# Kernel tuning notes

Hardware: AMD Instinct MI355X
Metric: run time of the kernel (lower is better)

## Reference

```python
import jax, jax.numpy as jnp
import numpy as np

B, N, C, H = 2, 2048, 1024, 16
D = C // H          # head_dim = 64
HALF = D // 2       # 32 complex pairs per head


def setup_inputs() -> dict:
    key = jax.random.key(0)
    k1, k2, k3, k4 = jax.random.split(key, 4)
    x = jax.random.normal(k1, (B, N, C), dtype=jnp.float32)
    # 0.02 init scale keeps softmax logits in a sane range
    qkv_w = jax.random.normal(k2, (3 * C, C), dtype=jnp.float32) * 0.02
    proj_w = jax.random.normal(k3, (C, C), dtype=jnp.float32) * 0.02
    proj_b = jax.random.normal(k4, (C,), dtype=jnp.float32) * 0.02
    # standard RoPE frequencies: theta = 10000^{-2i/D}
    inv_freq = 1.0 / (10000.0 ** (jnp.arange(0, D, 2, dtype=jnp.float32) / D))
    angles = jnp.arange(N, dtype=jnp.float32)[:, None] * inv_freq[None, :]  # [N, HALF]
    return {
        "x": x, "qkv_w": qkv_w, "proj_w": proj_w, "proj_b": proj_b,
        "freqs_cos": jnp.cos(angles), "freqs_sin": jnp.sin(angles),
    }


def _rope(t, cos, sin):
    # t: [B, N, H, D]; cos/sin: [N, HALF] -> broadcast as [1, N, 1, HALF]
    tr = t.reshape(B, N, H, HALF, 2)
    t_re, t_im = tr[..., 0], tr[..., 1]
    c = cos[None, :, None, :]
    s = sin[None, :, None, :]
    o_re = t_re * c - t_im * s
    o_im = t_re * s + t_im * c
    return jnp.stack([o_re, o_im], axis=-1).reshape(B, N, H, D)


def reference(x, qkv_w, proj_w, proj_b, freqs_cos, freqs_sin):
    scale = D ** -0.5
    qkv = x @ qkv_w.T                              # [B, N, 3C] (no bias: qkv_bias=False)
    qkv = qkv.reshape(B, N, 3, H, D)
    q, k, v = qkv[:, :, 0], qkv[:, :, 1], qkv[:, :, 2]  # [B, N, H, D]
    q = _rope(q, freqs_cos, freqs_sin)
    k = _rope(k, freqs_cos, freqs_sin)
    scores = jnp.einsum("bqhd,bkhd->bhqk", q, k) * scale
    attn = jax.nn.softmax(scores, axis=-1)         # dropout p=0.0 -> identity
    out = jnp.einsum("bhqk,bkhd->bqhd", attn, v).reshape(B, N, C)
    return out @ proj_w.T + proj_b
```

## Files before the change

### kernel.cpp

```cpp
#include <hip/hip_runtime.h>
#include <hip/hip_bf16.h>

#define B_ 2
#define N_ 2048
#define C_ 1024
#define H_ 16
#define D_ 64
#define HALF_ 32

typedef __attribute__((ext_vector_type(8))) __bf16 bf16x8;
typedef __attribute__((ext_vector_type(8))) unsigned short u16x8;
typedef __attribute__((ext_vector_type(4))) float f32x4;
typedef __attribute__((ext_vector_type(16))) float f32x16;

__device__ __forceinline__ unsigned short f2bf(float f) {
  union { float f; unsigned u; } v; v.f = f;
  unsigned r = v.u + 0x7FFFu + ((v.u >> 16) & 1u);
  return (unsigned short)(r >> 16);
}

__device__ __forceinline__ unsigned cvt_pk_bf16(float lo, float hi) {
  unsigned r;
  asm("v_cvt_pk_bf16_f32 %0, %1, %2" : "=v"(r) : "v"(lo), "v"(hi));
  return r;
}

__device__ __forceinline__ void gload_lds16(const void* g, void* l) {
  __builtin_amdgcn_global_load_lds(
      (const __attribute__((address_space(1))) void*)g,
      (__attribute__((address_space(3))) void*)l, 16, 0, 0);
}

__global__ __launch_bounds__(256) void cast3_f32_bf16(
    const float* __restrict__ a, const float* __restrict__ b,
    const float* __restrict__ c, unsigned short* __restrict__ oa,
    unsigned short* __restrict__ ob, unsigned short* __restrict__ oc,
    const float* __restrict__ cosT, const float* __restrict__ sinT,
    float2* __restrict__ csT) {
  int i = blockIdx.x * 256 + threadIdx.x;
  if (i >= 2097152) {
    int i2 = i - 2097152;
    csT[i2] = make_float2(cosT[i2], sinT[i2]);
    return;
  }
  const float4* src;
  ushort4* dst;
  int off;
  if (i < 1048576) {
    src = (const float4*)a; dst = (ushort4*)oa; off = i;
  } else if (i < 1835008) {
    src = (const float4*)b; dst = (ushort4*)ob; off = i - 1048576;
  } else {
    src = (const float4*)c; dst = (ushort4*)oc; off = i - 1835008;
  }
  float4 v = src[off];
  ushort4 o;
  o.x = f2bf(v.x); o.y = f2bf(v.y); o.z = f2bf(v.z); o.w = f2bf(v.w);
  dst[off] = o;
}

template <int EPI>
__global__ __launch_bounds__(256) void gemm_bt(
    const unsigned short* __restrict__ A, const unsigned short* __restrict__ Bw,
    int M, int Nn, int K,
    float* __restrict__ Cout, const float* __restrict__ bias,
    unsigned short* __restrict__ qo, unsigned short* __restrict__ ko,
    unsigned short* __restrict__ vto,
    const float2* __restrict__ csT) {
  __shared__ __align__(16) unsigned short As[2][128][64];
  __shared__ __align__(16) unsigned short Bs[2][128][64];
  const int tid = threadIdx.x;
  const int lane = tid & 63;
  const int wid = tid >> 6;
  const int wm = wid >> 1, wn = wid & 1;
  const int l15 = lane & 15;
  const int g = lane >> 4;

  const int per = gridDim.x >> 3;
  const int f = blockIdx.x;
  const int nat = (f & 7) * per + (f >> 3);
  const int mtiles = M >> 7;
  const int m0 = (nat % mtiles) * 128;
  const int n0 = (nat / mtiles) * 128;

  const int srow = wid * 8 + (lane >> 3);
  const int scol = ((lane & 7) ^ ((lane >> 3) & 7)) * 8;
  const int b7r = l15 & 7;

  auto stage = [&](int kt, int buf) {
#pragma unroll
    for (int j = 0; j < 4; ++j) {
      gload_lds16(&A[(size_t)(m0 + j * 32 + srow) * K + kt * 64 + scol],
                  &As[buf][j * 32 + wid * 8][0]);
      gload_lds16(&Bw[(size_t)(n0 + j * 32 + srow) * K + kt * 64 + scol],
                  &Bs[buf][j * 32 + wid * 8][0]);
    }
  };

  f32x4 acc[4][4] = {};

  const int nK = K >> 6;
  stage(0, 0);
  stage(1, 1);

  for (int kt = 0; kt < nK; ++kt) {
    const int buf = kt & 1;
    if (kt == nK - 1) asm volatile("s_waitcnt vmcnt(0)" ::: "memory");
    else              asm volatile("s_waitcnt vmcnt(8)" ::: "memory");
    __builtin_amdgcn_s_barrier();
    __builtin_amdgcn_sched_barrier(0);
#pragma unroll
    for (int kk = 0; kk < 2; ++kk) {
      bf16x8 af[4], bfv[4];
#pragma unroll
      for (int m = 0; m < 4; ++m)
        af[m] = *reinterpret_cast<const bf16x8*>(
            &As[buf][wm * 64 + m * 16 + l15][((kk * 4 + g) ^ b7r) * 8]);
#pragma unroll
      for (int n = 0; n < 4; ++n)
        bfv[n] = *reinterpret_cast<const bf16x8*>(
            &Bs[buf][wn * 64 + n * 16 + l15][((kk * 4 + g) ^ b7r) * 8]);
#pragma unroll
      for (int m = 0; m < 4; ++m)
#pragma unroll
        for (int n = 0; n < 4; ++n)
          acc[m][n] = __builtin_amdgcn_mfma_f32_16x16x32_bf16(af[m], bfv[n], acc[m][n], 0, 0, 0);
    }
    __builtin_amdgcn_s_barrier();
    if (kt + 2 < nK) stage(kt + 2, buf);
  }

  if constexpr (EPI == 0) {
#pragma unroll
    for (int n = 0; n < 4; ++n) {
      int col = n0 + wn * 64 + n * 16 + l15;
      float bv = bias[col];
#pragma unroll
      for (int m = 0; m < 4; ++m) {
        int rbase = m0 + wm * 64 + m * 16 + (lane >> 4) * 4;
#pragma unroll
        for (int r = 0; r < 4; ++r)
          Cout[(size_t)(rbase + r) * Nn + col] = acc[m][n][r] + bv;
      }
    }
  } else {
    const int which = n0 >> 10;
    if (which == 2) {
#pragma unroll
      for (int m = 0; m < 4; ++m)
#pragma unroll
        for (int n = 0; n < 4; ++n) {
          int col = n0 + wn * 64 + n * 16 + l15;
          int hc = col & 1023;
          int hh = hc >> 6, d = hc & 63;
          int row0 = m0 + wm * 64 + m * 16 + g * 4;
          int seq0 = row0 & (N_ - 1), bb = row0 >> 11;
          int seqP = (seq0 & ~12) | ((seq0 & 4) << 1) | ((seq0 & 8) >> 1);
          ushort4 pk;
          pk.x = f2bf(acc[m][n][0]); pk.y = f2bf(acc[m][n][1]);
          pk.z = f2bf(acc[m][n][2]); pk.w = f2bf(acc[m][n][3]);
          *reinterpret_cast<ushort4*>(
              &vto[(((size_t)bb * H_ + hh) * D_ + d) * N_ + seqP]) = pk;
        }
    } else {
      unsigned short* dst = (which == 0) ? qo : ko;
      const float qscale = (which == 0) ? 0.125f * 1.44269504f : 1.0f;
#pragma unroll
      for (int m = 0; m < 4; ++m)
#pragma unroll
        for (int n = 0; n < 4; ++n)
#pragma unroll
          for (int r = 0; r < 4; ++r) {
            int col = n0 + wn * 64 + n * 16 + l15;
            int row = m0 + wm * 64 + m * 16 + g * 4 + r;
            float val = acc[m][n][r];
            float partner = __shfl_xor(val, 1);
            int hc = col & 1023;
            int hh = hc >> 6, d = hc & 63;
            int seq = row & (N_ - 1), bb = row >> 11;
            float2 cs = csT[seq * HALF_ + (d >> 1)];
            float res = (d & 1) ? (partner * cs.y + val * cs.x) : (val * cs.x - partner * cs.y);
            res *= qscale;
            dst[(((size_t)bb * H_ + hh) * N_ + seq) * D_ + d] = f2bf(res);
          }
    }
  }
}

__global__ __launch_bounds__(512) void attn_kernel(
    const unsigned short* __restrict__ q,
    const unsigned short* __restrict__ k,
    const unsigned short* __restrict__ vt,
    unsigned short* __restrict__ o) {
  __shared__ __align__(16) unsigned short Kl[2][64][64];
  __shared__ __align__(16) unsigned short Vl[2][64][64];

  const int tid = threadIdx.x;
  const int lane = tid & 63;
  const int w = tid >> 6;
  const int l31 = lane & 31;
  const int hi = lane >> 5;

  const int bid = blockIdx.x;
  const int nat = (bid & 7) * 32 + (bid >> 3);
  const int qt = nat & 7;
  const int bh = nat >> 3;
  const int b = bh >> 4, h = bh & 15;

  const size_t hk = (size_t)bh * N_ * D_;
  const size_t hv = (size_t)bh * D_ * N_;
  const int qrow = qt * 256 + w * 32 + l31;

  bf16x8 qf[4];
#pragma unroll
  for (int kt = 0; kt < 4; ++kt)
    qf[kt] = *reinterpret_cast<const bf16x8*>(
        &q[hk + (size_t)qrow * D_ + kt * 16 + hi * 8]);

  const int prow = tid >> 3;
  const int pchk = tid & 7;
  const int swz = (pchk ^ (prow & 7)) * 8;

  u16x8 kr, vr;
  auto issueK = [&](int t) {
    kr = *reinterpret_cast<const u16x8*>(&k[hk + (size_t)(t * 64 + prow) * D_ + pchk * 8]);
  };
  auto issueV = [&](int t) {
    vr = *reinterpret_cast<const u16x8*>(&vt[hv + (size_t)prow * N_ + t * 64 + pchk * 8]);
  };
  auto commitK = [&](int buf) { *reinterpret_cast<u16x8*>(&Kl[buf][prow][swz]) = kr; };
  auto commitV = [&](int buf) { *reinterpret_cast<u16x8*>(&Vl[buf][prow][swz]) = vr; };

  f32x16 accO[2] = {};
  float lrun = 0.f;
  const int b7 = l31 & 7;
  const int NT = N_ / 64;

  f32x16 sA[2], sB[2];

#define QK_MFMA(T, SC)                                                        \
  do {                                                                        \
    f32x16 z_ = {};                                                           \
    SC[0] = z_; SC[1] = z_;                                                   \
    __builtin_amdgcn_s_setprio(1);                                            \
    _Pragma("unroll")                                                         \
    for (int kb = 0; kb < 2; ++kb)                                            \
      _Pragma("unroll")                                                       \
      for (int kt = 0; kt < 4; ++kt) {                                        \
        bf16x8 kf = *reinterpret_cast<const bf16x8*>(                         \
            &Kl[(T) & 1][kb * 32 + l31][(((kt * 2 + hi) ^ b7)) * 8]);         \
        SC[kb] = __builtin_amdgcn_mfma_f32_32x32x16_bf16(kf, qf[kt], SC[kb], 0, 0, 0); \
      }                                                                       \
    __builtin_amdgcn_s_setprio(0);                                            \
  } while (0)

#define SMPV(SP, VB)                                                          \
  do {                                                                        \
    _Pragma("unroll")                                                         \
    for (int kb = 0; kb < 2; ++kb)                                            \
      _Pragma("unroll")                                                       \
      for (int i = 0; i < 16; ++i) SP[kb][i] = __builtin_exp2f(SP[kb][i]);    \
    float sloc[16];                                                           \
    _Pragma("unroll")                                                         \
    for (int i = 0; i < 16; ++i) sloc[i] = SP[0][i] + SP[1][i];               \
    _Pragma("unroll")                                                         \
    for (int st = 8; st > 0; st >>= 1)                                        \
      _Pragma("unroll")                                                       \
      for (int i = 0; i < 8; ++i)                                             \
        if (i < st) sloc[i] += sloc[i + st];                                  \
    {                                                                         \
      unsigned ua = __float_as_uint(sloc[0]), ub = ua;                        \
      auto rr = __builtin_amdgcn_permlane32_swap(ua, ub, false, false);       \
      lrun += __uint_as_float(rr[0]) + __uint_as_float(rr[1]);                \
    }                                                                         \
    bf16x8 PA[4];                                                             \
    _Pragma("unroll")                                                         \
    for (int kvc = 0; kvc < 4; ++kvc) {                                       \
      const int kb = kvc >> 1, base = (kvc & 1) * 8;                          \
      union { unsigned u[4]; bf16x8 v; } pa;                                  \
      _Pragma("unroll")                                                       \
      for (int wd = 0; wd < 4; ++wd)                                          \
        pa.u[wd] = cvt_pk_bf16(SP[kb][base + 2 * wd], SP[kb][base + 2 * wd + 1]); \
      PA[kvc] = pa.v;                                                         \
    }                                                                         \
    __builtin_amdgcn_s_setprio(1);                                            \
    _Pragma("unroll")                                                         \
    for (int db = 0; db < 2; ++db)                                            \
      _Pragma("unroll")                                                       \
      for (int kvc = 0; kvc < 4; ++kvc) {                                     \
        bf16x8 vf = *reinterpret_cast<const bf16x8*>(                         \
            &Vl[VB][db * 32 + l31][(((kvc * 2 + hi) ^ b7)) * 8]);             \
        accO[db] = __builtin_amdgcn_mfma_f32_32x32x16_bf16(vf, PA[kvc], accO[db], 0, 0, 0); \
      }                                                                       \
    __builtin_amdgcn_s_setprio(0);                                            \
  } while (0)

#define BODY(T, SP, SC)                                                       \
  do {                                                                        \
    const int t_ = (T);                                                       \
    if (t_ + 1 < NT) issueK(t_ + 1);                                          \
    issueV(t_);                                                               \
    QK_MFMA(t_, SC);                                                          \
    SMPV(SP, (t_ - 1) & 1);                                                   \
    if (t_ + 1 < NT) commitK((t_ + 1) & 1);                                   \
    commitV(t_ & 1);                                                          \
    __syncthreads();                                                          \
  } while (0)

  issueK(0);
  commitK(0);
  __syncthreads();

  issueK(1);
  issueV(0);
  QK_MFMA(0, sA);
  commitK(1);
  commitV(0);
  __syncthreads();

  for (int tt = 1; tt + 1 < NT; tt += 2) {
    BODY(tt, sA, sB);
    BODY(tt + 1, sB, sA);
  }
  BODY(NT - 1, sA, sB);

  SMPV(sB, (NT - 1) & 1);

  float rl = 1.0f / lrun;
  const size_t obase = ((size_t)b * N_ + qrow) * C_ + h * 64;
#pragma unroll
  for (int db = 0; db < 2; ++db)
#pragma unroll
    for (int rg = 0; rg < 4; ++rg) {
      ushort4 pk;
      pk.x = f2bf(accO[db][rg * 4 + 0] * rl);
      pk.y = f2bf(accO[db][rg * 4 + 1] * rl);
      pk.z = f2bf(accO[db][rg * 4 + 2] * rl);
      pk.w = f2bf(accO[db][rg * 4 + 3] * rl);
      *reinterpret_cast<ushort4*>(&o[obase + db * 32 + rg * 8 + hi * 4]) = pk;
    }
#undef BODY
#undef SMPV
#undef QK_MFMA
}

extern "C" void kernel_launch(void* const* d_in, const int* in_sizes, int n_in,
                              void* d_out, int out_size, void* d_ws, size_t ws_size,
                              hipStream_t stream) {
  const float* x      = (const float*)d_in[0];
  const float* qkv_w  = (const float*)d_in[1];
  const float* proj_w = (const float*)d_in[2];
  const float* proj_b = (const float*)d_in[3];
  const float* cosT   = (const float*)d_in[4];
  const float* sinT   = (const float*)d_in[5];
  float* out = (float*)d_out;

  unsigned short* xb     = (unsigned short*)d_ws;
  unsigned short* wqkvb  = xb + (size_t)4096 * 1024;
  unsigned short* wprojb = wqkvb + (size_t)3072 * 1024;
  unsigned short* qb     = wprojb + (size_t)1024 * 1024;
  unsigned short* kb     = qb + (size_t)32 * 2048 * 64;
  unsigned short* vtb    = kb + (size_t)32 * 2048 * 64;
  unsigned short* ab     = vtb + (size_t)32 * 2048 * 64;
  float2* csT            = (float2*)(ab + (size_t)4096 * 1024);

  cast3_f32_bf16<<<8448, 256, 0, stream>>>(x, qkv_w, proj_w, xb, wqkvb, wprojb,
                                           cosT, sinT, csT);

  gemm_bt<1><<<768, 256, 0, stream>>>(xb, wqkvb, 4096, 3072, 1024,
                                      nullptr, nullptr, qb, kb, vtb, csT);

  attn_kernel<<<256, 512, 0, stream>>>(qb, kb, vtb, ab);

  gemm_bt<0><<<256, 256, 0, stream>>>(ab, wprojb, 4096, 1024, 1024,
                                      out, proj_b, nullptr, nullptr, nullptr,
                                      csT);
}
```

Measured before the change: 132.6 us.

## Split attention KV sequence across two wave groups per block with LDS combine

Doubles the attention block to 1024 threads, with two groups of 8 waves each processing half of the KV tiles for the same 256 query rows. Each group has its own K/V LDS buffers, and the partial O accumulators and row sums are merged through shared memory before normalisation. This raises parallelism and latency hiding, since the 256-block grid underfills the GPU. The costs are extra LDS, a combine step, and block-wide syncs across both groups. Exact max-free softmax makes the partial sums simply additive. A small cosmetic change in the GEMM epilogue swaps lane>>4 for g.

```diff
diff --git a/kernel.cpp b/kernel.cpp
--- a/kernel.cpp
+++ b/kernel.cpp
@@ -137,7 +137,7 @@
       float bv = bias[col];
 #pragma unroll
       for (int m = 0; m < 4; ++m) {
-        int rbase = m0 + wm * 64 + m * 16 + (lane >> 4) * 4;
+        int rbase = m0 + wm * 64 + m * 16 + g * 4;
 #pragma unroll
         for (int r = 0; r < 4; ++r)
           Cout[(size_t)(rbase + r) * Nn + col] = acc[m][n][r] + bv;
@@ -187,17 +187,20 @@
   }
 }
 
-__global__ __launch_bounds__(512) void attn_kernel(
+__global__ __launch_bounds__(1024, 4) void attn_kernel(
     const unsigned short* __restrict__ q,
     const unsigned short* __restrict__ k,
     const unsigned short* __restrict__ vt,
     unsigned short* __restrict__ o) {
-  __shared__ __align__(16) unsigned short Kl[2][64][64];
-  __shared__ __align__(16) unsigned short Vl[2][64][64];
+  __shared__ __align__(16) unsigned short Kl[2][2][64][64];
+  __shared__ __align__(16) unsigned short Vl[2][2][64][64];
+  __shared__ float comb[8][64][33];
 
   const int tid = threadIdx.x;
   const int lane = tid & 63;
   const int w = tid >> 6;
+  const int grp = w >> 3;
+  const int wg = w & 7;
   const int l31 = lane & 31;
   const int hi = lane >> 5;
 
@@ -209,7 +212,7 @@
 
   const size_t hk = (size_t)bh * N_ * D_;
   const size_t hv = (size_t)bh * D_ * N_;
-  const int qrow = qt * 256 + w * 32 + l31;
+  const int qrow = qt * 256 + wg * 32 + l31;
 
   bf16x8 qf[4];
 #pragma unroll
@@ -217,24 +220,28 @@
     qf[kt] = *reinterpret_cast<const bf16x8*>(
         &q[hk + (size_t)qrow * D_ + kt * 16 + hi * 8]);
 
-  const int prow = tid >> 3;
-  const int pchk = tid & 7;
+  const int stid = tid & 511;
+  const int prow = stid >> 3;
+  const int pchk = stid & 7;
   const int swz = (pchk ^ (prow & 7)) * 8;
+  const int NTG = 16;
+  const int t0 = grp * NTG;
 
   u16x8 kr, vr;
   auto issueK = [&](int t) {
-    kr = *reinterpret_cast<const u16x8*>(&k[hk + (size_t)(t * 64 + prow) * D_ + pchk * 8]);
+    kr = *reinterpret_cast<const u16x8*>(
+        &k[hk + (size_t)((t0 + t) * 64 + prow) * D_ + pchk * 8]);
   };
   auto issueV = [&](int t) {
-    vr = *reinterpret_cast<const u16x8*>(&vt[hv + (size_t)prow * N_ + t * 64 + pchk * 8]);
+    vr = *reinterpret_cast<const u16x8*>(
+        &vt[hv + (size_t)prow * N_ + (t0 + t) * 64 + pchk * 8]);
   };
-  auto commitK = [&](int buf) { *reinterpret_cast<u16x8*>(&Kl[buf][prow][swz]) = kr; };
-  auto commitV = [&](int buf) { *reinterpret_cast<u16x8*>(&Vl[buf][prow][swz]) = vr; };
+  auto commitK = [&](int buf) { *reinterpret_cast<u16x8*>(&Kl[grp][buf][prow][swz]) = kr; };
+  auto commitV = [&](int buf) { *reinterpret_cast<u16x8*>(&Vl[grp][buf][prow][swz]) = vr; };
 
   f32x16 accO[2] = {};
   float lrun = 0.f;
   const int b7 = l31 & 7;
-  const int NT = N_ / 64;
 
   f32x16 sA[2], sB[2];
 
@@ -248,7 +255,7 @@
       _Pragma("unroll")                                                       \
       for (int kt = 0; kt < 4; ++kt) {                                        \
         bf16x8 kf = *reinterpret_cast<const bf16x8*>(                         \
-            &Kl[(T) & 1][kb * 32 + l31][(((kt * 2 + hi) ^ b7)) * 8]);         \
+            &Kl[grp][(T) & 1][kb * 32 + l31][(((kt * 2 + hi) ^ b7)) * 8]);    \
         SC[kb] = __builtin_amdgcn_mfma_f32_32x32x16_bf16(kf, qf[kt], SC[kb], 0, 0, 0); \
       }                                                                       \
     __builtin_amdgcn_s_setprio(0);                                            \
@@ -289,7 +296,7 @@
       _Pragma("unroll")                                                       \
       for (int kvc = 0; kvc < 4; ++kvc) {                                     \
         bf16x8 vf = *reinterpret_cast<const bf16x8*>(                         \
-            &Vl[VB][db * 32 + l31][(((kvc * 2 + hi) ^ b7)) * 8]);             \
+            &Vl[grp][VB][db * 32 + l31][(((kvc * 2 + hi) ^ b7)) * 8]);        \
         accO[db] = __builtin_amdgcn_mfma_f32_32x32x16_bf16(vf, PA[kvc], accO[db], 0, 0, 0); \
       }                                                                       \
     __builtin_amdgcn_s_setprio(0);                                            \
@@ -298,11 +305,11 @@
 #define BODY(T, SP, SC)                                                       \
   do {                                                                        \
     const int t_ = (T);                                                       \
-    if (t_ + 1 < NT) issueK(t_ + 1);                                          \
+    if (t_ + 1 < NTG) issueK(t_ + 1);                                         \
     issueV(t_);                                                               \
     QK_MFMA(t_, SC);                                                          \
     SMPV(SP, (t_ - 1) & 1);                                                   \
-    if (t_ + 1 < NT) commitK((t_ + 1) & 1);                                   \
+    if (t_ + 1 < NTG) commitK((t_ + 1) & 1);                                  \
     commitV(t_ & 1);                                                          \
     __syncthreads();                                                          \
   } while (0)
@@ -318,27 +325,43 @@
   commitV(0);
   __syncthreads();
 
-  for (int tt = 1; tt + 1 < NT; tt += 2) {
+  for (int tt = 1; tt + 1 < NTG; tt += 2) {
     BODY(tt, sA, sB);
     BODY(tt + 1, sB, sA);
   }
-  BODY(NT - 1, sA, sB);
-
-  SMPV(sB, (NT - 1) & 1);
-
-  float rl = 1.0f / lrun;
-  const size_t obase = ((size_t)b * N_ + qrow) * C_ + h * 64;
-#pragma unroll
-  for (int db = 0; db < 2; ++db)
-#pragma unroll
-    for (int rg = 0; rg < 4; ++rg) {
-      ushort4 pk;
-      pk.x = f2bf(accO[db][rg * 4 + 0] * rl);
-      pk.y = f2bf(accO[db][rg * 4 + 1] * rl);
-      pk.z = f2bf(accO[db][rg * 4 + 2] * rl);
-      pk.w = f2bf(accO[db][rg * 4 + 3] * rl);
-      *reinterpret_cast<ushort4*>(&o[obase + db * 32 + rg * 8 + hi * 4]) = pk;
-    }
+  BODY(NTG - 1, sA, sB);
+
+  SMPV(sB, (NTG - 1) & 1);
+
+  if (grp == 1) {
+#pragma unroll
+    for (int db = 0; db < 2; ++db)
+#pragma unroll
+      for (int i = 0; i < 16; ++i) comb[wg][lane][db * 16 + i] = accO[db][i];
+    comb[wg][lane][32] = lrun;
+  }
+  __syncthreads();
+  if (grp == 0) {
+#pragma unroll
+    for (int db = 0; db < 2; ++db)
+#pragma unroll
+      for (int i = 0; i < 16; ++i) accO[db][i] += comb[wg][lane][db * 16 + i];
+    lrun += comb[wg][lane][32];
+
+    float rl = 1.0f / lrun;
+    const size_t obase = ((size_t)b * N_ + qrow) * C_ + h * 64;
+#pragma unroll
+    for (int db = 0; db < 2; ++db)
+#pragma unroll
+      for (int rg = 0; rg < 4; ++rg) {
+        ushort4 pk;
+        pk.x = f2bf(accO[db][rg * 4 + 0] * rl);
+        pk.y = f2bf(accO[db][rg * 4 + 1] * rl);
+        pk.z = f2bf(accO[db][rg * 4 + 2] * rl);
+        pk.w = f2bf(accO[db][rg * 4 + 3] * rl);
+        *reinterpret_cast<ushort4*>(&o[obase + db * 32 + rg * 8 + hi * 4]) = pk;
+      }
+  }
 #undef BODY
 #undef SMPV
 #undef QK_MFMA
@@ -370,7 +393,7 @@
   gemm_bt<1><<<768, 256, 0, stream>>>(xb, wqkvb, 4096, 3072, 1024,
                                       nullptr, nullptr, qb, kb, vtb, csT);
 
-  attn_kernel<<<256, 512, 0, stream>>>(qb, kb, vtb, ab);
+  attn_kernel<<<256, 1024, 0, stream>>>(qb, kb, vtb, ab);
 
   gemm_bt<0><<<256, 256, 0, stream>>>(ab, wprojb, 4096, 1024, 1024,
                                       out, proj_b, nullptr, nullptr, nullptr,
```

Result: slower. 246.0 us (+85.5%).

## Process two KV tiles per iteration with four-deep LDS ring buffer

Applied to the files above, without the earlier changes.

The attention loop now loads and commits K and V for two 64-key tiles at once into a 4-slot LDS ring, then runs both QK MFMA blocks, followed by both softmax/PV steps. This halves the number of block-wide barriers and gives longer independent MFMA runs between global loads and LDS commits. The cost is double the LDS footprint (64KB), which may reduce occupancy, plus more live registers for the extra staged loads and score tiles. The previous software pipeline, where QK of the next tile overlapped the softmax of the current one, is replaced by a simpler grouped ordering. A minor epilogue index change in the GEMM uses g instead of lane>>4.

```diff
diff --git a/kernel.cpp b/kernel.cpp
--- a/kernel.cpp
+++ b/kernel.cpp
@@ -137,7 +137,7 @@
       float bv = bias[col];
 #pragma unroll
       for (int m = 0; m < 4; ++m) {
-        int rbase = m0 + wm * 64 + m * 16 + (lane >> 4) * 4;
+        int rbase = m0 + wm * 64 + m * 16 + g * 4;
 #pragma unroll
         for (int r = 0; r < 4; ++r)
           Cout[(size_t)(rbase + r) * Nn + col] = acc[m][n][r] + bv;
@@ -192,8 +192,8 @@
     const unsigned short* __restrict__ k,
     const unsigned short* __restrict__ vt,
     unsigned short* __restrict__ o) {
-  __shared__ __align__(16) unsigned short Kl[2][64][64];
-  __shared__ __align__(16) unsigned short Vl[2][64][64];
+  __shared__ __align__(16) unsigned short Kl[4][64][64];
+  __shared__ __align__(16) unsigned short Vl[4][64][64];
 
   const int tid = threadIdx.x;
   const int lane = tid & 63;
@@ -221,15 +221,23 @@
   const int pchk = tid & 7;
   const int swz = (pchk ^ (prow & 7)) * 8;
 
-  u16x8 kr, vr;
-  auto issueK = [&](int t) {
-    kr = *reinterpret_cast<const u16x8*>(&k[hk + (size_t)(t * 64 + prow) * D_ + pchk * 8]);
-  };
-  auto issueV = [&](int t) {
-    vr = *reinterpret_cast<const u16x8*>(&vt[hv + (size_t)prow * N_ + t * 64 + pchk * 8]);
-  };
-  auto commitK = [&](int buf) { *reinterpret_cast<u16x8*>(&Kl[buf][prow][swz]) = kr; };
-  auto commitV = [&](int buf) { *reinterpret_cast<u16x8*>(&Vl[buf][prow][swz]) = vr; };
+  u16x8 kr0, vr0, kr1, vr1;
+  auto issue0 = [&](int t) {
+    kr0 = *reinterpret_cast<const u16x8*>(&k[hk + (size_t)(t * 64 + prow) * D_ + pchk * 8]);
+    vr0 = *reinterpret_cast<const u16x8*>(&vt[hv + (size_t)prow * N_ + t * 64 + pchk * 8]);
+  };
+  auto issue1 = [&](int t) {
+    kr1 = *reinterpret_cast<const u16x8*>(&k[hk + (size_t)(t * 64 + prow) * D_ + pchk * 8]);
+    vr1 = *reinterpret_cast<const u16x8*>(&vt[hv + (size_t)prow * N_ + t * 64 + pchk * 8]);
+  };
+  auto commit0 = [&](int buf) {
+    *reinterpret_cast<u16x8*>(&Kl[buf][prow][swz]) = kr0;
+    *reinterpret_cast<u16x8*>(&Vl[buf][prow][swz]) = vr0;
+  };
+  auto commit1 = [&](int buf) {
+    *reinterpret_cast<u16x8*>(&Kl[buf][prow][swz]) = kr1;
+    *reinterpret_cast<u16x8*>(&Vl[buf][prow][swz]) = vr1;
+  };
 
   f32x16 accO[2] = {};
   float lrun = 0.f;
@@ -238,7 +246,7 @@
 
   f32x16 sA[2], sB[2];
 
-#define QK_MFMA(T, SC)                                                        \
+#define QK_MFMA(BUF, SC)                                                      \
   do {                                                                        \
     f32x16 z_ = {};                                                           \
     SC[0] = z_; SC[1] = z_;                                                   \
@@ -248,7 +256,7 @@
       _Pragma("unroll")                                                       \
       for (int kt = 0; kt < 4; ++kt) {                                        \
         bf16x8 kf = *reinterpret_cast<const bf16x8*>(                         \
-            &Kl[(T) & 1][kb * 32 + l31][(((kt * 2 + hi) ^ b7)) * 8]);         \
+            &Kl[BUF][kb * 32 + l31][(((kt * 2 + hi) ^ b7)) * 8]);             \
         SC[kb] = __builtin_amdgcn_mfma_f32_32x32x16_bf16(kf, qf[kt], SC[kb], 0, 0, 0); \
       }                                                                       \
     __builtin_amdgcn_s_setprio(0);                                            \
@@ -295,36 +303,25 @@
     __builtin_amdgcn_s_setprio(0);                                            \
   } while (0)
 
-#define BODY(T, SP, SC)                                                       \
-  do {                                                                        \
-    const int t_ = (T);                                                       \
-    if (t_ + 1 < NT) issueK(t_ + 1);                                          \
-    issueV(t_);                                                               \
-    QK_MFMA(t_, SC);                                                          \
-    SMPV(SP, (t_ - 1) & 1);                                                   \
-    if (t_ + 1 < NT) commitK((t_ + 1) & 1);                                   \
-    commitV(t_ & 1);                                                          \
-    __syncthreads();                                                          \
-  } while (0)
-
-  issueK(0);
-  commitK(0);
+  issue0(0);
+  commit0(0);
+  issue1(1);
+  commit1(1);
   __syncthreads();
 
-  issueK(1);
-  issueV(0);
-  QK_MFMA(0, sA);
-  commitK(1);
-  commitV(0);
-  __syncthreads();
-
-  for (int tt = 1; tt + 1 < NT; tt += 2) {
-    BODY(tt, sA, sB);
-    BODY(tt + 1, sB, sA);
-  }
-  BODY(NT - 1, sA, sB);
-
-  SMPV(sB, (NT - 1) & 1);
+  for (int tt = 0; tt < NT; tt += 2) {
+    const bool more = (tt + 2 < NT);
+    if (more) { issue0(tt + 2); issue1(tt + 3); }
+    QK_MFMA(tt & 3, sA);
+    QK_MFMA((tt + 1) & 3, sB);
+    SMPV(sA, tt & 3);
+    SMPV(sB, (tt + 1) & 3);
+    if (more) {
+      commit0((tt + 2) & 3);
+      commit1((tt + 3) & 3);
+      __syncthreads();
+    }
+  }
 
   float rl = 1.0f / lrun;
   const size_t obase = ((size_t)b * N_ + qrow) * C_ + h * 64;
@@ -339,7 +336,6 @@
       pk.w = f2bf(accO[db][rg * 4 + 3] * rl);
       *reinterpret_cast<ushort4*>(&o[obase + db * 32 + rg * 8 + hi * 4]) = pk;
     }
-#undef BODY
 #undef SMPV
 #undef QK_MFMA
 }
```

Result: slower. 135.3 us (+2.0%).
